# Performance work log

Measured on AMD Instinct MI355X. Metric: run time of the kernel, lower is better.

Reference implementation:

```python
import jax, jax.numpy as jnp
import numpy as np

T_HORIZON = 1.0
REG = 0.01


def setup_inputs() -> dict:
    key = jax.random.key(0)
    kx, = jax.random.split(key, 1)
    B, N = 2, 8192
    # sorted event times in [0, 1); horizon T = 1.0 > all events
    x = jnp.sort(jax.random.uniform(kx, (B, N), dtype=jnp.float32), axis=-1)
    mu = jnp.full((1,), 0.5, dtype=jnp.float32)
    alpha = jnp.full((1,), 0.5, dtype=jnp.float32)
    w = jnp.full((1,), 1.0, dtype=jnp.float32)
    return {"x": x, "mu": mu, "alpha": alpha, "w": w}


def reference(x, mu, alpha, w):
    # x: [B, N] event times; mu/alpha/w: shape (1,) Hawkes parameters
    # delta[b, i, j] = x[b, j] - x[b, i]
    delta = x[:, None, :] - x[:, :, None]                       # [B, N, N]
    # masked_fill(delta <= 0, -inf) then exp -> exactly zero on non-causal pairs
    kern = jnp.exp(-w * jnp.where(delta > 0, delta, jnp.inf))   # [B, N, N]
    # sum over dim=1 (i.e. over past events i for each event j)
    excite = alpha * w * jnp.sum(kern, axis=1)                  # [B, N]
    pos = jnp.log(mu + excite)                                  # [B, N]
    neg = alpha * (1.0 - jnp.exp(-w * (T_HORIZON - x)))         # [B, N]
    nll = mu * T_HORIZON - jnp.sum(pos) + jnp.sum(neg)          # shape (1,)
    loss = nll + REG * (-jnp.log(mu) - jnp.log(alpha) - jnp.log(w))
    return loss
```

## Files before the change

### kernel.cpp

```cpp
#include <hip/hip_runtime.h>
#include <math.h>


#define BLOCK 1024
#define ITEMS 8
#define NWAVES (BLOCK / 64)

__launch_bounds__(BLOCK)
__global__ void hawkes_nll_kernel(const float* __restrict__ x,
                                  const float* __restrict__ mu_p,
                                  const float* __restrict__ alpha_p,
                                  const float* __restrict__ w_p,
                                  float* __restrict__ out,
                                  int B) {
    const float mu    = mu_p[0];
    const float alpha = alpha_p[0];
    const float w     = w_p[0];
    const float aw    = alpha * w;

    const int tid  = threadIdx.x;
    const int lane = tid & 63;
    const int wave = tid >> 6;

    __shared__ float  s_wave[NWAVES];
    __shared__ double s_pos[NWAVES];
    __shared__ double s_neg[NWAVES];

    double pos_sum = 0.0;
    double neg_sum = 0.0;

    const int N = BLOCK * ITEMS;

    for (int b = 0; b < B; ++b) {
        const float* xb = x + (size_t)b * N;
        const int base = tid * ITEMS;

        float xs[ITEMS];
        float ys[ITEMS];
        float tsum = 0.0f;
#pragma unroll
        for (int i = 0; i < ITEMS; ++i) {
            xs[i] = xb[base + i];
            ys[i] = __expf(w * xs[i]);
            tsum += ys[i];
        }

        float v = tsum;
#pragma unroll
        for (int off = 1; off < 64; off <<= 1) {
            float n = __shfl_up(v, off, 64);
            if (lane >= off) v += n;
        }
        if (lane == 63) s_wave[wave] = v;
        __syncthreads();
        if (wave == 0) {
            float t = (lane < NWAVES) ? s_wave[lane] : 0.0f;
#pragma unroll
            for (int off = 1; off < NWAVES; off <<= 1) {
                float n = __shfl_up(t, off, 64);
                if (lane >= off) t += n;
            }
            if (lane < NWAVES) s_wave[lane] = t;
        }
        __syncthreads();
        float run = ((wave == 0) ? 0.0f : s_wave[wave - 1]) + (v - tsum);

#pragma unroll
        for (int i = 0; i < ITEMS; ++i) {
            float S = __expf(-w * xs[i]) * run;
            pos_sum += (double)__logf(mu + aw * S);
            neg_sum += (double)(alpha * (1.0f - __expf(-w * (1.0f - xs[i]))));
            run += ys[i];
        }
        __syncthreads();
    }

#pragma unroll
    for (int off = 32; off > 0; off >>= 1) {
        pos_sum += __shfl_down(pos_sum, off, 64);
        neg_sum += __shfl_down(neg_sum, off, 64);
    }
    if (lane == 0) { s_pos[wave] = pos_sum; s_neg[wave] = neg_sum; }
    __syncthreads();
    if (tid == 0) {
        double P = 0.0, Ng = 0.0;
#pragma unroll
        for (int i = 0; i < NWAVES; ++i) { P += s_pos[i]; Ng += s_neg[i]; }
        const double T_HORIZON = 1.0;
        const double REG = 0.01;
        double nll = (double)mu * T_HORIZON - P + Ng;
        double loss = nll + REG * (-log((double)mu) - log((double)alpha) - log((double)w));
        out[0] = (float)loss;
    }
}

extern "C" void kernel_launch(void* const* d_in, const int* in_sizes, int n_in,
                              void* d_out, int out_size, void* d_ws, size_t ws_size,
                              hipStream_t stream) {
    const float* x     = (const float*)d_in[0];
    const float* mu    = (const float*)d_in[1];
    const float* alpha = (const float*)d_in[2];
    const float* w     = (const float*)d_in[3];
    float* out = (float*)d_out;

    const int N = BLOCK * ITEMS;
    const int B = in_sizes[0] / N;

    hipLaunchKernelGGL(hawkes_nll_kernel, dim3(1), dim3(BLOCK), 0, stream,
                       x, mu, alpha, w, out, B);
}
```

Baseline: 64.20 us.

## Split single-block scan into multi-block three-kernel scan with atomic reduction

Replaces the single 1024-thread block that loops over batches with a three-kernel pipeline. The first kernel computes per-chunk sums of exp(w*x), the second scans within each chunk with a serial prefix over earlier chunk sums, and the third combines atomically accumulated double sums into the loss. This spreads work across many CUs instead of one and rewrites exp(-w*(1-x)) as exp(-w)*y to drop exponentials. It adds two extra kernel launches and uses S = prefix/y, which relies on exp(w*x) staying well-conditioned in float32.

```diff
diff --git a/kernel.cpp b/kernel.cpp
--- a/kernel.cpp
+++ b/kernel.cpp
@@ -2,94 +2,106 @@
 #include <math.h>
 
 
-#define BLOCK 1024
-#define ITEMS 8
-#define NWAVES (BLOCK / 64)
+#define BS 256
+#define CHUNK 256
+#define NWAVE (BS / 64)
 
-__launch_bounds__(BLOCK)
-__global__ void hawkes_nll_kernel(const float* __restrict__ x,
-                                  const float* __restrict__ mu_p,
-                                  const float* __restrict__ alpha_p,
-                                  const float* __restrict__ w_p,
-                                  float* __restrict__ out,
-                                  int B) {
-    const float mu    = mu_p[0];
-    const float alpha = alpha_p[0];
-    const float w     = w_p[0];
-    const float aw    = alpha * w;
+__launch_bounds__(BS)
+__global__ void k1_bsums(const float* __restrict__ x,
+                         const float* __restrict__ w_p,
+                         float* __restrict__ bsums,
+                         double* __restrict__ acc,
+                         int NB, int N) {
+    const float w = w_p[0];
+    const int blk = blockIdx.x;
+    const int row = blk / NB, cblk = blk - row * NB;
+    const int tid = threadIdx.x, lane = tid & 63, wave = tid >> 6;
 
-    const int tid  = threadIdx.x;
-    const int lane = tid & 63;
-    const int wave = tid >> 6;
+    const float y = __expf(w * x[(size_t)row * N + cblk * CHUNK + tid]);
 
-    __shared__ float  s_wave[NWAVES];
-    __shared__ double s_pos[NWAVES];
-    __shared__ double s_neg[NWAVES];
+    float v = y;
+#pragma unroll
+    for (int off = 32; off > 0; off >>= 1) v += __shfl_down(v, off, 64);
 
-    double pos_sum = 0.0;
-    double neg_sum = 0.0;
+    __shared__ float sw[NWAVE];
+    if (lane == 0) sw[wave] = v;
+    __syncthreads();
+    if (tid == 0) {
+        float t = 0.0f;
+#pragma unroll
+        for (int i = 0; i < NWAVE; ++i) t += sw[i];
+        bsums[blk] = t;
+        if (blk == 0) { acc[0] = 0.0; acc[1] = 0.0; }
+    }
+}
 
-    const int N = BLOCK * ITEMS;
+__launch_bounds__(BS)
+__global__ void k2_main(const float* __restrict__ x,
+                        const float* __restrict__ mu_p,
+                        const float* __restrict__ alpha_p,
+                        const float* __restrict__ w_p,
+                        const float* __restrict__ bsums,
+                        double* __restrict__ acc,
+                        int NB, int N) {
+    const float mu = mu_p[0], alpha = alpha_p[0], w = w_p[0];
+    const float aw = alpha * w;
+    const float cneg = __expf(-w);
 
-    for (int b = 0; b < B; ++b) {
-        const float* xb = x + (size_t)b * N;
-        const int base = tid * ITEMS;
+    const int blk = blockIdx.x;
+    const int row = blk / NB, cblk = blk - row * NB;
+    const int tid = threadIdx.x, lane = tid & 63, wave = tid >> 6;
 
-        float xs[ITEMS];
-        float ys[ITEMS];
-        float tsum = 0.0f;
+    const float y = __expf(w * x[(size_t)row * N + cblk * CHUNK + tid]);
+
+    float base = 0.0f;
+    for (int i = 0; i < cblk; ++i) base += bsums[row * NB + i];
+
+    float v = y;
 #pragma unroll
-        for (int i = 0; i < ITEMS; ++i) {
-            xs[i] = xb[base + i];
-            ys[i] = __expf(w * xs[i]);
-            tsum += ys[i];
-        }
+    for (int off = 1; off < 64; off <<= 1) {
+        float n = __shfl_up(v, off, 64);
+        if (lane >= off) v += n;
+    }
+    __shared__ float sw[NWAVE];
+    if (lane == 63) sw[wave] = v;
+    __syncthreads();
+    float woff = 0.0f;
+#pragma unroll
+    for (int i = 0; i < NWAVE; ++i) if (i < wave) woff += sw[i];
+    const float prefix = base + woff + (v - y);
 
-        float v = tsum;
-#pragma unroll
-        for (int off = 1; off < 64; off <<= 1) {
-            float n = __shfl_up(v, off, 64);
-            if (lane >= off) v += n;
-        }
-        if (lane == 63) s_wave[wave] = v;
-        __syncthreads();
-        if (wave == 0) {
-            float t = (lane < NWAVES) ? s_wave[lane] : 0.0f;
-#pragma unroll
-            for (int off = 1; off < NWAVES; off <<= 1) {
-                float n = __shfl_up(t, off, 64);
-                if (lane >= off) t += n;
-            }
-            if (lane < NWAVES) s_wave[lane] = t;
-        }
-        __syncthreads();
-        float run = ((wave == 0) ? 0.0f : s_wave[wave - 1]) + (v - tsum);
+    const float S   = prefix / y;
+    const float pos = __logf(mu + aw * S);
+    const float neg = alpha * (1.0f - cneg * y);
 
-#pragma unroll
-        for (int i = 0; i < ITEMS; ++i) {
-            float S = __expf(-w * xs[i]) * run;
-            pos_sum += (double)__logf(mu + aw * S);
-            neg_sum += (double)(alpha * (1.0f - __expf(-w * (1.0f - xs[i]))));
-            run += ys[i];
-        }
-        __syncthreads();
-    }
-
+    double pd = (double)pos, nd = (double)neg;
 #pragma unroll
     for (int off = 32; off > 0; off >>= 1) {
-        pos_sum += __shfl_down(pos_sum, off, 64);
-        neg_sum += __shfl_down(neg_sum, off, 64);
+        pd += __shfl_down(pd, off, 64);
+        nd += __shfl_down(nd, off, 64);
     }
-    if (lane == 0) { s_pos[wave] = pos_sum; s_neg[wave] = neg_sum; }
+    __shared__ double sp[NWAVE], sn[NWAVE];
+    if (lane == 0) { sp[wave] = pd; sn[wave] = nd; }
     __syncthreads();
     if (tid == 0) {
         double P = 0.0, Ng = 0.0;
 #pragma unroll
-        for (int i = 0; i < NWAVES; ++i) { P += s_pos[i]; Ng += s_neg[i]; }
-        const double T_HORIZON = 1.0;
-        const double REG = 0.01;
-        double nll = (double)mu * T_HORIZON - P + Ng;
-        double loss = nll + REG * (-log((double)mu) - log((double)alpha) - log((double)w));
+        for (int i = 0; i < NWAVE; ++i) { P += sp[i]; Ng += sn[i]; }
+        atomicAdd(&acc[0], P);
+        atomicAdd(&acc[1], Ng);
+    }
+}
+
+__global__ void k3_final(const float* __restrict__ mu_p,
+                         const float* __restrict__ alpha_p,
+                         const float* __restrict__ w_p,
+                         const double* __restrict__ acc,
+                         float* __restrict__ out) {
+    if (threadIdx.x == 0 && blockIdx.x == 0) {
+        const double mu = mu_p[0], alpha = alpha_p[0], w = w_p[0];
+        const double T_HORIZON = 1.0, REG = 0.01;
+        double loss = mu * T_HORIZON - acc[0] + acc[1]
+                    + REG * (-log(mu) - log(alpha) - log(w));
         out[0] = (float)loss;
     }
 }
@@ -103,9 +115,18 @@
     const float* w     = (const float*)d_in[3];
     float* out = (float*)d_out;
 
-    const int N = BLOCK * ITEMS;
-    const int B = in_sizes[0] / N;
+    const int N  = 8192;
+    const int B  = in_sizes[0] / N;
+    const int NB = N / CHUNK;
+    const int nblk = B * NB;
 
-    hipLaunchKernelGGL(hawkes_nll_kernel, dim3(1), dim3(BLOCK), 0, stream,
-                       x, mu, alpha, w, out, B);
+    double* acc   = (double*)d_ws;
+    float*  bsums = (float*)(acc + 2);
+
+    hipLaunchKernelGGL(k1_bsums, dim3(nblk), dim3(BS), 0, stream,
+                       x, w, bsums, acc, NB, N);
+    hipLaunchKernelGGL(k2_main, dim3(nblk), dim3(BS), 0, stream,
+                       x, mu, alpha, w, bsums, acc, NB, N);
+    hipLaunchKernelGGL(k3_final, dim3(1), dim3(64), 0, stream,
+                       mu, alpha, w, acc, out);
 }
```

Result: no change. 65.17 us (+1.5%).
